# Performance work log

Measured on AMD Instinct MI355X. Metric: run time of the kernel, lower is better.

The kernel has to match this reference:

```python
import jax, jax.numpy as jnp
import numpy as np

B, S, R, H, NH, HD = 32, 1026, 256, 1024, 16, 64

def setup_inputs() -> dict:
    key = jax.random.key(0)
    ks = jax.random.split(key, 8)
    sc = 0.02
    return {
        "q_low": jax.random.normal(ks[0], (B, S, R), jnp.float32),
        "k_low": jax.random.normal(ks[1], (B, S, R), jnp.float32),
        "v_low": jax.random.normal(ks[2], (B, S, R), jnp.float32),
        "Wq": jax.random.normal(ks[3], (R, H), jnp.float32) * sc,
        "bq": jnp.zeros((H,), jnp.float32),
        "Wk": jax.random.normal(ks[4], (R, H), jnp.float32) * sc,
        "bk": jnp.zeros((H,), jnp.float32),
        "Wv": jax.random.normal(ks[5], (R, H), jnp.float32) * sc,
        "bv": jnp.zeros((H,), jnp.float32),
        "Wo_down": jax.random.normal(ks[6], (H, R), jnp.float32) * sc,
    }

def reference(q_low, k_low, v_low, Wq, bq, Wk, bk, Wv, bv, Wo_down):
    # Up-project low-rank activations to full Q, K, V: [B,S,R] @ [R,H] -> [B,S,H]
    q = q_low @ Wq + bq
    k = k_low @ Wk + bk
    v = v_low @ Wv + bv
    # split heads: [B,S,NH,HD] -> [B,NH,S,HD]
    def split(x):
        return x.reshape(B, S, NH, HD).transpose(0, 2, 1, 3)
    qh, kh, vh = split(q), split(k), split(v)
    scores = jnp.einsum('bhqd,bhkd->bhqk', qh, kh) / jnp.sqrt(jnp.float32(HD))
    probs = jax.nn.softmax(scores, axis=-1)  # dropout p=0
    ctx = jnp.einsum('bhqk,bhkd->bhqd', probs, vh)
    ctx = ctx.transpose(0, 2, 1, 3).reshape(B, S, H)
    # Down-project with low-rank activation (gelu)
    out_low = jax.nn.gelu(ctx @ Wo_down, approximate=False)
    return out_low
```

## Files before the change

kernel.cpp:

```cpp
#include <hip/hip_runtime.h>
#include <hip/hip_bf16.h>
#include <math.h>

using short8   = __attribute__((ext_vector_type(8))) short;
using floatx4  = __attribute__((ext_vector_type(4))) float;
using floatx16 = __attribute__((ext_vector_type(16))) float;

#define B_N  32
#define S_N  1026
#define R_N  256
#define H_N  1024
#define NH_N 16
#define HD_N 64
#define SP_N 1088
#define KTILES 17
#define CS_LD 136

__device__ __forceinline__ float bf2f(__hip_bfloat16 x) { return __bfloat162float(x); }
__device__ __forceinline__ __hip_bfloat16 f2bf(float x) { return __float2bfloat16(x); }

__device__ __forceinline__ float fast_exp2(float x) {
#if __has_builtin(__builtin_amdgcn_exp2f)
    return __builtin_amdgcn_exp2f(x);
#else
    return exp2f(x);
#endif
}

__device__ __forceinline__ unsigned cvtpk(float lo, float hi_) {
    unsigned r;
    asm("v_cvt_pk_bf16_f32 %0, %1, %2" : "=v"(r) : "v"(lo), "v"(hi_));
    return r;
}

__device__ __forceinline__ void gl_lds16(const void* g, void* l) {
    __builtin_amdgcn_global_load_lds(
        (const __attribute__((address_space(1))) unsigned int*)g,
        (__attribute__((address_space(3))) unsigned int*)l, 16, 0, 0);
}

__device__ __forceinline__ int xcd_swz(int o, int nwg) {
    return ((nwg & 7) == 0) ? ((o & 7) * (nwg >> 3) + (o >> 3)) : o;
}

__device__ __forceinline__ short8 cvt8(const float* __restrict__ p) {
    floatx4 a = *(const floatx4*)p;
    floatx4 b = *(const floatx4*)(p + 4);
    short8 o;
    __hip_bfloat16* op = (__hip_bfloat16*)&o;
    op[0] = f2bf(a[0]); op[1] = f2bf(a[1]); op[2] = f2bf(a[2]); op[3] = f2bf(a[3]);
    op[4] = f2bf(b[0]); op[5] = f2bf(b[1]); op[6] = f2bf(b[2]); op[7] = f2bf(b[3]);
    return o;
}

__global__ __launch_bounds__(256) void transpose3_kernel(
    const float* __restrict__ a, const float* __restrict__ b, const float* __restrict__ c,
    __hip_bfloat16* __restrict__ oa, __hip_bfloat16* __restrict__ ob,
    __hip_bfloat16* __restrict__ oc, int K, int N) {
    __shared__ __hip_bfloat16 t[32][33];
    const float* in = (blockIdx.z == 0) ? a : (blockIdx.z == 1) ? b : c;
    __hip_bfloat16* out = (blockIdx.z == 0) ? oa : (blockIdx.z == 1) ? ob : oc;
    const int k0 = blockIdx.x * 32, n0 = blockIdx.y * 32;
    const int tx = threadIdx.x & 31, ty = threadIdx.x >> 5;
#pragma unroll
    for (int j = 0; j < 32; j += 8)
        t[ty + j][tx] = f2bf(in[(size_t)(k0 + ty + j) * N + n0 + tx]);
    __syncthreads();
#pragma unroll
    for (int j = 0; j < 32; j += 8)
        out[(size_t)(n0 + ty + j) * K + k0 + tx] = t[tx][ty + j];
}

__global__ __launch_bounds__(256) void transpose_kernel(const float* __restrict__ in,
                                                        __hip_bfloat16* __restrict__ out,
                                                        int K, int N) {
    __shared__ __hip_bfloat16 t[32][33];
    const int k0 = blockIdx.x * 32, n0 = blockIdx.y * 32;
    const int tx = threadIdx.x & 31, ty = threadIdx.x >> 5;
#pragma unroll
    for (int j = 0; j < 32; j += 8)
        t[ty + j][tx] = f2bf(in[(size_t)(k0 + ty + j) * N + n0 + tx]);
    __syncthreads();
#pragma unroll
    for (int j = 0; j < 32; j += 8)
        out[(size_t)(n0 + ty + j) * K + k0 + tx] = t[tx][ty + j];
}

__global__ __launch_bounds__(256) void cvtx_kernel(
    const float* __restrict__ q, const float* __restrict__ k, const float* __restrict__ v,
    __hip_bfloat16* __restrict__ oq, __hip_bfloat16* __restrict__ ok,
    __hip_bfloat16* __restrict__ ov, int n8) {
    int idx = blockIdx.x * 256 + threadIdx.x;
    if (idx >= n8) return;
    const float* s = (blockIdx.y == 0) ? q : (blockIdx.y == 1) ? k : v;
    __hip_bfloat16* d = (blockIdx.y == 0) ? oq : (blockIdx.y == 1) ? ok : ov;
    *(short8*)(d + (size_t)idx * 8) = cvt8(s + (size_t)idx * 8);
}

__global__ void padv_kernel(__hip_bfloat16* __restrict__ Vt, int total) {
    int idx = blockIdx.x * 256 + threadIdx.x;
    if (idx < total) {
        int p  = idx % (SP_N - S_N);
        int rd = idx / (SP_N - S_N);
        Vt[(size_t)rd * SP_N + S_N + p] = f2bf(0.f);
    }
}

__global__ __launch_bounds__(256) void qkvproj_kernel(
    const __hip_bfloat16* __restrict__ Xq, const __hip_bfloat16* __restrict__ Xk,
    const __hip_bfloat16* __restrict__ Xv,
    const __hip_bfloat16* __restrict__ WqT, const __hip_bfloat16* __restrict__ WkT,
    const __hip_bfloat16* __restrict__ WvT,
    const float* __restrict__ bq, const float* __restrict__ bk,
    const float* __restrict__ bv,
    __hip_bfloat16* __restrict__ Qc, __hip_bfloat16* __restrict__ Kc,
    __hip_bfloat16* __restrict__ Vc, int Mc, float qscale) {
    __shared__ char smem[34816];
    typedef __hip_bfloat16 (*AB_t)[128][32];
    AB_t As = (AB_t)smem;
    AB_t Bs = (AB_t)(smem + 16384);
    __hip_bfloat16* Cs = (__hip_bfloat16*)smem;

    const int nx = gridDim.x;
    const int nwg = nx * 8 * 3;
    const int o = blockIdx.x + nx * (blockIdx.y + 8 * blockIdx.z);
    const int tlin = xcd_swz(o, nwg);
    const int ty = tlin & 7;
    const int rest = tlin >> 3;
    const int tx = rest % nx, tz = rest / nx;

    const __hip_bfloat16* X  = (tz == 0) ? Xq  : (tz == 1) ? Xk  : Xv;
    const __hip_bfloat16* WT = (tz == 0) ? WqT : (tz == 1) ? WkT : WvT;
    const float* bias        = (tz == 0) ? bq  : (tz == 1) ? bk  : bv;
    __hip_bfloat16* out      = (tz == 0) ? Qc  : (tz == 1) ? Kc  : Vc;
    const float oscale = (tz == 0) ? qscale : 1.0f;
    const int mode = (tz == 2);

    const int tid  = threadIdx.x;
    const int wave = tid >> 6, lane = tid & 63;
    const int quad = lane >> 4, l16 = lane & 15;
    const int tm = tx * 128, tn = ty * 128;
    const int mw = (wave >> 1) * 64, nw = (wave & 1) * 64;
    const int lr = lane >> 2;
    const int sc4 = (lane & 3) ^ (lr & 3);

    floatx4 acc[4][4] = {};

    auto stage = [&](int bb, int kk) {
#pragma unroll
        for (int s16 = 0; s16 < 2; ++s16) {
            int row = wave * 32 + s16 * 16;
            int gm = tm + row + lr; if (gm >= Mc) gm = Mc - 1;
            gl_lds16(X + (size_t)gm * R_N + kk + sc4 * 8, &As[bb][row][0]);
            gl_lds16(WT + (size_t)(tn + row + lr) * R_N + kk + sc4 * 8, &Bs[bb][row][0]);
        }
    };

    stage(0, 0);
    __syncthreads();

    for (int t = 0; t < R_N / 32; ++t) {
        const int bb = t & 1;
        if (t + 1 < R_N / 32) stage(bb ^ 1, (t + 1) * 32);
        short8 af[4], bfr[4];
#pragma unroll
        for (int mb = 0; mb < 4; ++mb) {
            int row = mw + mb * 16 + l16;
            af[mb] = *(const short8*)((const char*)&As[bb][row][0] + ((quad ^ (row & 3)) << 4));
        }
#pragma unroll
        for (int nb = 0; nb < 4; ++nb) {
            int row = nw + nb * 16 + l16;
            bfr[nb] = *(const short8*)((const char*)&Bs[bb][row][0] + ((quad ^ (row & 3)) << 4));
        }
        if (mode == 0) {
#pragma unroll
            for (int mb = 0; mb < 4; ++mb)
#pragma unroll
                for (int nb = 0; nb < 4; ++nb)
                    acc[mb][nb] = __builtin_amdgcn_mfma_f32_16x16x32_bf16(af[mb], bfr[nb], acc[mb][nb], 0, 0, 0);
        } else {
#pragma unroll
            for (int mb = 0; mb < 4; ++mb)
#pragma unroll
                for (int nb = 0; nb < 4; ++nb)
                    acc[mb][nb] = __builtin_amdgcn_mfma_f32_16x16x32_bf16(bfr[nb], af[mb], acc[mb][nb], 0, 0, 0);
        }
        __syncthreads();
    }

    if (mode == 0) {
#pragma unroll
        for (int mb = 0; mb < 4; ++mb)
#pragma unroll
            for (int nb = 0; nb < 4; ++nb) {
                int j = nw + nb * 16 + l16;
                float bv_ = bias[tn + j];
#pragma unroll
                for (int r = 0; r < 4; ++r) {
                    int i = mw + mb * 16 + quad * 4 + r;
                    Cs[i * CS_LD + j] = f2bf(oscale * (acc[mb][nb][r] + bv_));
                }
            }
    } else {
#pragma unroll
        for (int mb = 0; mb < 4; ++mb)
#pragma unroll
            for (int nb = 0; nb < 4; ++nb)
#pragma unroll
                for (int r = 0; r < 4; ++r) {
                    int i = nw + nb * 16 + quad * 4 + r;
                    int j = mw + mb * 16 + l16;
                    Cs[i * CS_LD + j] = f2bf(acc[mb][nb][r] + bias[tn + i]);
                }
    }
    __syncthreads();

    const int i = tid >> 1, half = tid & 1;
    if (mode == 0) {
        int m = tm + i;
        if (m < Mc) {
            int bl = m / S_N, s = m - bl * S_N;
            int h = (tn >> 6) + half;
            size_t ob = ((size_t)((bl * NH_N + h) * S_N + s)) * HD_N;
            const __hip_bfloat16* src = Cs + i * CS_LD + half * 64;
#pragma unroll
            for (int j = 0; j < 8; ++j)
                *(short8*)(out + ob + j * 8) = *(const short8*)(src + j * 8);
        }
    } else {
        int n = tn + i;
        int h = n >> 6, d = n & 63;
        const __hip_bfloat16* src = Cs + i * CS_LD + half * 64;
#pragma unroll
        for (int j = 0; j < 8; ++j) {
            int m0 = tm + half * 64 + j * 8;
            if (m0 >= Mc) continue;
            short8 w = *(const short8*)(src + j * 8);
            int bl = m0 / S_N, s0 = m0 - bl * S_N;
            size_t ob = ((size_t)((bl * NH_N + h) * HD_N + d)) * SP_N;
            if (s0 + 8 <= S_N) {
                const unsigned* wp = (const unsigned*)&w;
#pragma unroll
                for (int k = 0; k < 4; ++k)
                    *(unsigned*)(out + ob + s0 + 2 * k) = wp[k];
            } else {
                const __hip_bfloat16* we = (const __hip_bfloat16*)&w;
#pragma unroll
                for (int e = 0; e < 8; ++e) {
                    int m = m0 + e;
                    int bl2 = m / S_N, s2 = m - bl2 * S_N;
                    out[((size_t)((bl2 * NH_N + h) * HD_N + d)) * SP_N + s2] = we[e];
                }
            }
        }
    }
}

__global__ __launch_bounds__(256, 3) void attn_kernel(
    const __hip_bfloat16* __restrict__ Qh,
    const __hip_bfloat16* __restrict__ Kh,
    const __hip_bfloat16* __restrict__ Vt,
    __hip_bfloat16* __restrict__ ctx) {
    __shared__ __hip_bfloat16 Kl[2][64][64];
    __shared__ __hip_bfloat16 Vl[2][64][64];

    const int ny = gridDim.y;
    const int nwg = gridDim.x * ny;
    const int o = blockIdx.x + gridDim.x * blockIdx.y;
    const int tlin = xcd_swz(o, nwg);
    const int bh = tlin / ny;
    const int q0 = (tlin % ny) * 128;

    const int tid = threadIdx.x;
    const int wave = tid >> 6, lane = tid & 63;
    const int c = lane & 31, hi = lane >> 5, c7 = c & 7;
    const size_t base  = (size_t)bh * S_N * HD_N;
    const size_t vbase = (size_t)bh * HD_N * SP_N;

    const int lr = lane >> 3;
    const int sc = (lane & 7) ^ lr;

    const short ONE = 0x3F80;
    const short8 onesb = {ONE, ONE, ONE, ONE, ONE, ONE, ONE, ONE};

    short8 qf[4];
    {
        int qrow = q0 + wave * 32 + c;
        if (qrow > S_N - 1) qrow = S_N - 1;
        const __hip_bfloat16* qp = Qh + base + (size_t)qrow * HD_N + hi * 8;
#pragma unroll
        for (int i = 0; i < 4; ++i) qf[i] = *(const short8*)(qp + 16 * i);
    }

    floatx16 oacc[2] = {};
    floatx16 rsacc = {};

    auto stage = [&](int bb, int kt) {
#pragma unroll
        for (int j = 0; j < 2; ++j) {
            int r = 16 * wave + 8 * j + lr;
            int krow = kt + r;
            if (krow > S_N - 1) krow = S_N - 1;
            gl_lds16(Kh + base + (size_t)krow * HD_N + sc * 8,
                     &Kl[bb][16 * wave + 8 * j][0]);
            gl_lds16(Vt + vbase + (size_t)r * SP_N + kt + sc * 8,
                     &Vl[bb][16 * wave + 8 * j][0]);
        }
    };

    stage(0, 0);
    __syncthreads();

    int bb = 0;
    for (int t = 0; t < KTILES; ++t) {
        const int kt = t * 64;
        if (t + 1 < KTILES) stage(bb ^ 1, kt + 64);
        const bool last = (kt + 64 > S_N);

        short8 pa[2][2];
#pragma unroll
        for (int sub = 0; sub < 2; ++sub) {
            floatx16 sacc = {};
            __builtin_amdgcn_s_setprio(1);
#pragma unroll
            for (int i = 0; i < 4; ++i) {
                short8 kf = *(const short8*)&Kl[bb][32 * sub + c][(((2 * i + hi) ^ c7) << 3)];
                sacc = __builtin_amdgcn_mfma_f32_32x32x16_bf16(kf, qf[i], sacc, 0, 0, 0);
            }
            __builtin_amdgcn_s_setprio(0);
            float ps[16];
            if (!last) {
#pragma unroll
                for (int r = 0; r < 16; ++r) ps[r] = fast_exp2(sacc[r]);
            } else {
#pragma unroll
                for (int r = 0; r < 16; ++r) {
                    int key = kt + 32 * sub + (r & 3) + 8 * (r >> 2) + 4 * hi;
                    ps[r] = (key < S_N) ? fast_exp2(sacc[r]) : 0.f;
                }
            }
#pragma unroll
            for (int step = 0; step < 2; ++step) {
                unsigned w0 = cvtpk(ps[8 * step + 0], ps[8 * step + 1]);
                unsigned w1 = cvtpk(ps[8 * step + 2], ps[8 * step + 3]);
                unsigned w2 = cvtpk(ps[8 * step + 4], ps[8 * step + 5]);
                unsigned w3 = cvtpk(ps[8 * step + 6], ps[8 * step + 7]);
                asm("v_permlane32_swap_b32 %0, %1" : "+v"(w0), "+v"(w2));
                asm("v_permlane32_swap_b32 %0, %1" : "+v"(w1), "+v"(w3));
                union { unsigned u[4]; short8 s; } fu;
                fu.u[0] = w0; fu.u[1] = w1; fu.u[2] = w2; fu.u[3] = w3;
                pa[sub][step] = fu.s;
            }
        }

        __builtin_amdgcn_s_setprio(1);
#pragma unroll
        for (int db = 0; db < 2; ++db)
#pragma unroll
            for (int sub = 0; sub < 2; ++sub)
#pragma unroll
                for (int step = 0; step < 2; ++step) {
                    short8 vf = *(const short8*)
                        &Vl[bb][32 * db + c][((((sub * 2 + step) * 2 + hi) ^ c7) << 3)];
                    oacc[db] = __builtin_amdgcn_mfma_f32_32x32x16_bf16(pa[sub][step], vf, oacc[db], 0, 0, 0);
                }
#pragma unroll
        for (int sub = 0; sub < 2; ++sub)
#pragma unroll
            for (int step = 0; step < 2; ++step)
                rsacc = __builtin_amdgcn_mfma_f32_32x32x16_bf16(pa[sub][step], onesb, rsacc, 0, 0, 0);
        __builtin_amdgcn_s_setprio(0);

        __syncthreads();
        bb ^= 1;
    }

    const int bl = bh / NH_N, h = bh - bl * NH_N;
    const int srow0 = q0 + wave * 32;
#pragma unroll
    for (int r = 0; r < 16; ++r) {
        int q = (r & 3) + 8 * (r >> 2) + 4 * hi;
        int s = srow0 + q;
        if (s < S_N) {
            float rr = 1.0f / rsacc[r];
            size_t o2 = ((size_t)(bl * S_N + s)) * H_N + h * HD_N + c;
            ctx[o2]      = f2bf(oacc[0][r] * rr);
            ctx[o2 + 32] = f2bf(oacc[1][r] * rr);
        }
    }
}

__global__ __launch_bounds__(256) void dproj_kernel(
    const __hip_bfloat16* __restrict__ X,
    const __hip_bfloat16* __restrict__ WT,
    float* __restrict__ out,
    int Mc) {
    __shared__ char smem[49152];
    typedef __hip_bfloat16 (*A_t)[64][64];
    typedef __hip_bfloat16 (*B_t)[128][64];
    A_t As = (A_t)smem;
    B_t Bs = (B_t)(smem + 16384);
    float* Csf = (float*)smem;

    const int nx = (Mc + 63) >> 6;
    const int tlin = xcd_swz(blockIdx.x, gridDim.x);
    if (tlin >= nx * 2) return;
    const int ty = tlin & 1, tx = tlin >> 1;

    const int tid  = threadIdx.x;
    const int wave = tid >> 6, lane = tid & 63;
    const int quad = lane >> 4, l16 = lane & 15;
    const int tm = tx * 64, tn = ty * 128;
    const int mw = (wave >> 1) * 32, nw = (wave & 1) * 64;
    const int lr = lane >> 3;
    const int sc = (lane & 7) ^ lr;

    floatx4 acc[2][4] = {};

    auto stage = [&](int bb, int kk) {
#pragma unroll
        for (int s8 = 0; s8 < 2; ++s8) {
            int row = wave * 16 + s8 * 8;
            int gm = tm + row + lr; if (gm >= Mc) gm = Mc - 1;
            gl_lds16(X + (size_t)gm * H_N + kk + sc * 8, &As[bb][row][0]);
        }
#pragma unroll
        for (int s8 = 0; s8 < 4; ++s8) {
            int row = wave * 32 + s8 * 8;
            gl_lds16(WT + (size_t)(tn + row + lr) * H_N + kk + sc * 8, &Bs[bb][row][0]);
        }
    };

    stage(0, 0);
    __syncthreads();

    for (int t = 0; t < H_N / 64; ++t) {
        const int bb = t & 1;
        if (t + 1 < H_N / 64) stage(bb ^ 1, (t + 1) * 64);
        short8 af[2][2], bfr[4][2];
#pragma unroll
        for (int mb = 0; mb < 2; ++mb) {
            int row = mw + mb * 16 + l16;
            const char* rp = (const char*)&As[bb][row][0];
#pragma unroll
            for (int k2 = 0; k2 < 2; ++k2)
                af[mb][k2] = *(const short8*)(rp + ((((k2 * 4 + quad)) ^ (row & 7)) << 4));
        }
#pragma unroll
        for (int nb = 0; nb < 4; ++nb) {
            int row = nw + nb * 16 + l16;
            const char* rp = (const char*)&Bs[bb][row][0];
#pragma unroll
            for (int k2 = 0; k2 < 2; ++k2)
                bfr[nb][k2] = *(const short8*)(rp + ((((k2 * 4 + quad)) ^ (row & 7)) << 4));
        }
#pragma unroll
        for (int mb = 0; mb < 2; ++mb)
#pragma unroll
            for (int nb = 0; nb < 4; ++nb) {
                acc[mb][nb] = __builtin_amdgcn_mfma_f32_16x16x32_bf16(af[mb][0], bfr[nb][0], acc[mb][nb], 0, 0, 0);
                acc[mb][nb] = __builtin_amdgcn_mfma_f32_16x16x32_bf16(af[mb][1], bfr[nb][1], acc[mb][nb], 0, 0, 0);
            }
        __syncthreads();
    }

#pragma unroll
    for (int mb = 0; mb < 2; ++mb)
#pragma unroll
        for (int nb = 0; nb < 4; ++nb)
#pragma unroll
            for (int r = 0; r < 4; ++r) {
                int i = mw + mb * 16 + quad * 4 + r;
                int j = nw + nb * 16 + l16;
                float x = acc[mb][nb][r];
                Csf[i * CS_LD + j] = 0.5f * x * (1.0f + erff(x * 0.70710678118654752f));
            }
    __syncthreads();

    {
        const int i = tid >> 2, q32 = tid & 3;
        int m = tm + i;
        if (m < Mc) {
            const float* src = Csf + i * CS_LD + q32 * 32;
            float* dst = out + (size_t)m * R_N + tn + q32 * 32;
#pragma unroll
            for (int jj = 0; jj < 8; ++jj)
                *(floatx4*)(dst + jj * 4) = *(const floatx4*)(src + jj * 4);
        }
    }
}

extern "C" void kernel_launch(void* const* d_in, const int* in_sizes, int n_in,
                              void* d_out, int out_size, void* d_ws, size_t ws_size,
                              hipStream_t stream) {
    const float* q_low = (const float*)d_in[0];
    const float* k_low = (const float*)d_in[1];
    const float* v_low = (const float*)d_in[2];
    const float* Wq    = (const float*)d_in[3];
    const float* bq    = (const float*)d_in[4];
    const float* Wk    = (const float*)d_in[5];
    const float* bk    = (const float*)d_in[6];
    const float* Wv    = (const float*)d_in[7];
    const float* bv    = (const float*)d_in[8];
    const float* Wo    = (const float*)d_in[9];
    float* out = (float*)d_out;
    (void)in_sizes; (void)n_in; (void)out_size;

    const float QSCALE = 0.125f * 1.44269504088896f;
    const size_t SZ_W = (size_t)H_N * R_N * 2;

    int C = 32;
    while (C > 1) {
        size_t qk = (size_t)C * NH_N * S_N * HD_N * 2;
        size_t vv = (size_t)C * NH_N * HD_N * SP_N * 2;
        size_t cx = (size_t)C * S_N * H_N * 2;
        if (4 * SZ_W + 2 * qk + vv + cx <= ws_size) break;
        C >>= 1;
    }

    char* ws = (char*)d_ws;
    const size_t SZ_QK = (size_t)C * NH_N * S_N * HD_N * 2;
    const size_t SZ_V  = (size_t)C * NH_N * HD_N * SP_N * 2;
    __hip_bfloat16* WqT = (__hip_bfloat16*)(ws);
    __hip_bfloat16* WkT = (__hip_bfloat16*)(ws + SZ_W);
    __hip_bfloat16* WvT = (__hip_bfloat16*)(ws + 2 * SZ_W);
    __hip_bfloat16* WoT = (__hip_bfloat16*)(ws + 3 * SZ_W);
    __hip_bfloat16* Qc  = (__hip_bfloat16*)(ws + 4 * SZ_W);
    __hip_bfloat16* Kc  = (__hip_bfloat16*)(ws + 4 * SZ_W + SZ_QK);
    __hip_bfloat16* Vc  = (__hip_bfloat16*)(ws + 4 * SZ_W + 2 * SZ_QK);
    __hip_bfloat16* ctc = (__hip_bfloat16*)(ws + 4 * SZ_W + 2 * SZ_QK + SZ_V);

    {
        dim3 tg(R_N / 32, H_N / 32, 3);
        transpose3_kernel<<<tg, 256, 0, stream>>>(Wq, Wk, Wv, WqT, WkT, WvT, R_N, H_N);
        dim3 to(H_N / 32, R_N / 32);
        transpose_kernel<<<to, 256, 0, stream>>>(Wo, WoT, H_N, R_N);
    }

    {
        int total = C * NH_N * HD_N * (SP_N - S_N);
        padv_kernel<<<(total + 255) / 256, 256, 0, stream>>>(Vc, total);
    }

    for (int c0 = 0; c0 < B_N; c0 += C) {
        const int Mc = C * S_N;
        const size_t xoff = (size_t)c0 * S_N * R_N;

        __hip_bfloat16* Xq = ctc;
        __hip_bfloat16* Xk = ctc + (size_t)Mc * R_N;
        __hip_bfloat16* Xv = ctc + 2 * (size_t)Mc * R_N;
        {
            int n8 = Mc * R_N / 8;
            dim3 cg((n8 + 255) / 256, 3);
            cvtx_kernel<<<cg, 256, 0, stream>>>(q_low + xoff, k_low + xoff, v_low + xoff,
                                                Xq, Xk, Xv, n8);
        }

        dim3 pg((Mc + 127) / 128, H_N / 128, 3);
        qkvproj_kernel<<<pg, 256, 0, stream>>>(Xq, Xk, Xv, WqT, WkT, WvT,
                                               bq, bk, bv, Qc, Kc, Vc, Mc, QSCALE);

        dim3 ag(C * NH_N, (S_N + 127) / 128);
        attn_kernel<<<ag, 256, 0, stream>>>(Qc, Kc, Vc, ctc);

        int nxd = (Mc + 63) / 64;
        int dg1 = ((nxd * 2 + 7) / 8) * 8;
        dproj_kernel<<<dg1, 256, 0, stream>>>(ctc, WoT, out + xoff, Mc);
    }
}
```

Baseline: 518.1 us.

## Process two query tiles per wave in attention to reuse K/V LDS fragments

The attention kernel now uses 2 waves (128 threads) per block instead of 4. Each wave handles 64 query rows as two 32-row groups, so every K and V fragment read from LDS feeds two MFMAs instead of one. Each wave also stages twice as many K/V rows. This halves LDS read traffic per query row and raises MFMA density. The cost is doubled accumulator and register pressure, fewer waves per block to hide latency, and launch bounds that change occupancy.

```diff
diff --git a/kernel.cpp b/kernel.cpp
--- a/kernel.cpp
+++ b/kernel.cpp
@@ -257,7 +257,7 @@
     }
 }
 
-__global__ __launch_bounds__(256, 3) void attn_kernel(
+__global__ __launch_bounds__(128, 2) void attn_kernel(
     const __hip_bfloat16* __restrict__ Qh,
     const __hip_bfloat16* __restrict__ Kh,
     const __hip_bfloat16* __restrict__ Vt,
@@ -284,28 +284,29 @@
     const short ONE = 0x3F80;
     const short8 onesb = {ONE, ONE, ONE, ONE, ONE, ONE, ONE, ONE};
 
-    short8 qf[4];
-    {
-        int qrow = q0 + wave * 32 + c;
+    short8 qf[2][4];
+#pragma unroll
+    for (int g = 0; g < 2; ++g) {
+        int qrow = q0 + wave * 64 + g * 32 + c;
         if (qrow > S_N - 1) qrow = S_N - 1;
         const __hip_bfloat16* qp = Qh + base + (size_t)qrow * HD_N + hi * 8;
 #pragma unroll
-        for (int i = 0; i < 4; ++i) qf[i] = *(const short8*)(qp + 16 * i);
-    }
-
-    floatx16 oacc[2] = {};
-    floatx16 rsacc = {};
+        for (int i = 0; i < 4; ++i) qf[g][i] = *(const short8*)(qp + 16 * i);
+    }
+
+    floatx16 oacc[2][2] = {};
+    floatx16 rsacc[2] = {};
 
     auto stage = [&](int bb, int kt) {
 #pragma unroll
-        for (int j = 0; j < 2; ++j) {
-            int r = 16 * wave + 8 * j + lr;
+        for (int j = 0; j < 4; ++j) {
+            int r = 32 * wave + 8 * j + lr;
             int krow = kt + r;
             if (krow > S_N - 1) krow = S_N - 1;
             gl_lds16(Kh + base + (size_t)krow * HD_N + sc * 8,
-                     &Kl[bb][16 * wave + 8 * j][0]);
+                     &Kl[bb][32 * wave + 8 * j][0]);
             gl_lds16(Vt + vbase + (size_t)r * SP_N + kt + sc * 8,
-                     &Vl[bb][16 * wave + 8 * j][0]);
+                     &Vl[bb][32 * wave + 8 * j][0]);
         }
     };
 
@@ -318,39 +319,44 @@
         if (t + 1 < KTILES) stage(bb ^ 1, kt + 64);
         const bool last = (kt + 64 > S_N);
 
-        short8 pa[2][2];
+        short8 pa[2][2][2];
 #pragma unroll
         for (int sub = 0; sub < 2; ++sub) {
-            floatx16 sacc = {};
-            __builtin_amdgcn_s_setprio(1);
-#pragma unroll
-            for (int i = 0; i < 4; ++i) {
-                short8 kf = *(const short8*)&Kl[bb][32 * sub + c][(((2 * i + hi) ^ c7) << 3)];
-                sacc = __builtin_amdgcn_mfma_f32_32x32x16_bf16(kf, qf[i], sacc, 0, 0, 0);
-            }
-            __builtin_amdgcn_s_setprio(0);
-            float ps[16];
-            if (!last) {
-#pragma unroll
-                for (int r = 0; r < 16; ++r) ps[r] = fast_exp2(sacc[r]);
-            } else {
-#pragma unroll
-                for (int r = 0; r < 16; ++r) {
-                    int key = kt + 32 * sub + (r & 3) + 8 * (r >> 2) + 4 * hi;
-                    ps[r] = (key < S_N) ? fast_exp2(sacc[r]) : 0.f;
+            short8 kf[4];
+#pragma unroll
+            for (int i = 0; i < 4; ++i)
+                kf[i] = *(const short8*)&Kl[bb][32 * sub + c][(((2 * i + hi) ^ c7) << 3)];
+#pragma unroll
+            for (int g = 0; g < 2; ++g) {
+                floatx16 sacc = {};
+                __builtin_amdgcn_s_setprio(1);
+#pragma unroll
+                for (int i = 0; i < 4; ++i)
+                    sacc = __builtin_amdgcn_mfma_f32_32x32x16_bf16(kf[i], qf[g][i], sacc, 0, 0, 0);
+                __builtin_amdgcn_s_setprio(0);
+                float ps[16];
+                if (!last) {
+#pragma unroll
+                    for (int r = 0; r < 16; ++r) ps[r] = fast_exp2(sacc[r]);
+                } else {
+#pragma unroll
+                    for (int r = 0; r < 16; ++r) {
+                        int key = kt + 32 * sub + (r & 3) + 8 * (r >> 2) + 4 * hi;
+                        ps[r] = (key < S_N) ? fast_exp2(sacc[r]) : 0.f;
+                    }
                 }
-            }
-#pragma unroll
-            for (int step = 0; step < 2; ++step) {
-                unsigned w0 = cvtpk(ps[8 * step + 0], ps[8 * step + 1]);
-                unsigned w1 = cvtpk(ps[8 * step + 2], ps[8 * step + 3]);
-                unsigned w2 = cvtpk(ps[8 * step + 4], ps[8 * step + 5]);
-                unsigned w3 = cvtpk(ps[8 * step + 6], ps[8 * step + 7]);
-                asm("v_permlane32_swap_b32 %0, %1" : "+v"(w0), "+v"(w2));
-                asm("v_permlane32_swap_b32 %0, %1" : "+v"(w1), "+v"(w3));
-                union { unsigned u[4]; short8 s; } fu;
-                fu.u[0] = w0; fu.u[1] = w1; fu.u[2] = w2; fu.u[3] = w3;
-                pa[sub][step] = fu.s;
+#pragma unroll
+                for (int step = 0; step < 2; ++step) {
+                    unsigned w0 = cvtpk(ps[8 * step + 0], ps[8 * step + 1]);
+                    unsigned w1 = cvtpk(ps[8 * step + 2], ps[8 * step + 3]);
+                    unsigned w2 = cvtpk(ps[8 * step + 4], ps[8 * step + 5]);
+                    unsigned w3 = cvtpk(ps[8 * step + 6], ps[8 * step + 7]);
+                    asm("v_permlane32_swap_b32 %0, %1" : "+v"(w0), "+v"(w2));
+                    asm("v_permlane32_swap_b32 %0, %1" : "+v"(w1), "+v"(w3));
+                    union { unsigned u[4]; short8 s; } fu;
+                    fu.u[0] = w0; fu.u[1] = w1; fu.u[2] = w2; fu.u[3] = w3;
+                    pa[g][sub][step] = fu.s;
+                }
             }
         }
 
@@ -363,13 +369,17 @@
                 for (int step = 0; step < 2; ++step) {
                     short8 vf = *(const short8*)
                         &Vl[bb][32 * db + c][((((sub * 2 + step) * 2 + hi) ^ c7) << 3)];
-                    oacc[db] = __builtin_amdgcn_mfma_f32_32x32x16_bf16(pa[sub][step], vf, oacc[db], 0, 0, 0);
+#pragma unroll
+                    for (int g = 0; g < 2; ++g)
+                        oacc[g][db] = __builtin_amdgcn_mfma_f32_32x32x16_bf16(pa[g][sub][step], vf, oacc[g][db], 0, 0, 0);
                 }
 #pragma unroll
         for (int sub = 0; sub < 2; ++sub)
 #pragma unroll
             for (int step = 0; step < 2; ++step)
-                rsacc = __builtin_amdgcn_mfma_f32_32x32x16_bf16(pa[sub][step], onesb, rsacc, 0, 0, 0);
+#pragma unroll
+                for (int g = 0; g < 2; ++g)
+                    rsacc[g] = __builtin_amdgcn_mfma_f32_32x32x16_bf16(pa[g][sub][step], onesb, rsacc[g], 0, 0, 0);
         __builtin_amdgcn_s_setprio(0);
 
         __syncthreads();
@@ -377,16 +387,19 @@
     }
 
     const int bl = bh / NH_N, h = bh - bl * NH_N;
-    const int srow0 = q0 + wave * 32;
-#pragma unroll
-    for (int r = 0; r < 16; ++r) {
-        int q = (r & 3) + 8 * (r >> 2) + 4 * hi;
-        int s = srow0 + q;
-        if (s < S_N) {
-            float rr = 1.0f / rsacc[r];
-            size_t o2 = ((size_t)(bl * S_N + s)) * H_N + h * HD_N + c;
-            ctx[o2]      = f2bf(oacc[0][r] * rr);
-            ctx[o2 + 32] = f2bf(oacc[1][r] * rr);
+#pragma unroll
+    for (int g = 0; g < 2; ++g) {
+        const int srow0 = q0 + wave * 64 + g * 32;
+#pragma unroll
+        for (int r = 0; r < 16; ++r) {
+            int q = (r & 3) + 8 * (r >> 2) + 4 * hi;
+            int s = srow0 + q;
+            if (s < S_N) {
+                float rr = 1.0f / rsacc[g][r];
+                size_t o2 = ((size_t)(bl * S_N + s)) * H_N + h * HD_N + c;
+                ctx[o2]      = f2bf(oacc[g][0][r] * rr);
+                ctx[o2 + 32] = f2bf(oacc[g][1][r] * rr);
+            }
         }
     }
 }
@@ -562,7 +575,7 @@
                                                bq, bk, bv, Qc, Kc, Vc, Mc, QSCALE);
 
         dim3 ag(C * NH_N, (S_N + 127) / 128);
-        attn_kernel<<<ag, 256, 0, stream>>>(Qc, Kc, Vc, ctc);
+        attn_kernel<<<ag, 128, 0, stream>>>(Qc, Kc, Vc, ctc);
 
         int nxd = (Mc + 63) / 64;
         int dg1 = ((nxd * 2 + 7) / 8) * 8;
```

Measured after the change: 557.9 us. 7.7% more time.

## Enlarge QKV projection tile to 256x128 with 512-thread blocks

Applied to the files above, without the earlier changes.

The QKV up-projection GEMM now uses 256-row M tiles and 8 waves per block, so each staged weight (B) tile is reused across twice as many activation rows. To fit the larger A tile in shared memory, the epilogue writes results through the C staging buffer in two passes of 128 rows each, with extra barriers. This cuts redundant weight loads and the block count, at the cost of more LDS per block, possible lower occupancy, and a serialized two-pass epilogue.

```diff
diff --git a/kernel.cpp b/kernel.cpp
--- a/kernel.cpp
+++ b/kernel.cpp
@@ -106,7 +106,7 @@
     }
 }
 
-__global__ __launch_bounds__(256) void qkvproj_kernel(
+__global__ __launch_bounds__(512) void qkvproj_kernel(
     const __hip_bfloat16* __restrict__ Xq, const __hip_bfloat16* __restrict__ Xk,
     const __hip_bfloat16* __restrict__ Xv,
     const __hip_bfloat16* __restrict__ WqT, const __hip_bfloat16* __restrict__ WkT,
@@ -115,10 +115,11 @@
     const float* __restrict__ bv,
     __hip_bfloat16* __restrict__ Qc, __hip_bfloat16* __restrict__ Kc,
     __hip_bfloat16* __restrict__ Vc, int Mc, float qscale) {
-    __shared__ char smem[34816];
-    typedef __hip_bfloat16 (*AB_t)[128][32];
-    AB_t As = (AB_t)smem;
-    AB_t Bs = (AB_t)(smem + 16384);
+    __shared__ char smem[49152];
+    typedef __hip_bfloat16 (*A_t)[256][32];
+    typedef __hip_bfloat16 (*B_t)[128][32];
+    A_t As = (A_t)smem;
+    B_t Bs = (B_t)(smem + 32768);
     __hip_bfloat16* Cs = (__hip_bfloat16*)smem;
 
     const int nx = gridDim.x;
@@ -139,8 +140,9 @@
     const int tid  = threadIdx.x;
     const int wave = tid >> 6, lane = tid & 63;
     const int quad = lane >> 4, l16 = lane & 15;
-    const int tm = tx * 128, tn = ty * 128;
-    const int mw = (wave >> 1) * 64, nw = (wave & 1) * 64;
+    const int tm = tx * 256, tn = ty * 128;
+    const int wm = wave >> 1, wn = wave & 1;
+    const int mw = wm * 64, nw = wn * 64;
     const int lr = lane >> 2;
     const int sc4 = (lane & 3) ^ (lr & 3);
 
@@ -152,6 +154,9 @@
             int row = wave * 32 + s16 * 16;
             int gm = tm + row + lr; if (gm >= Mc) gm = Mc - 1;
             gl_lds16(X + (size_t)gm * R_N + kk + sc4 * 8, &As[bb][row][0]);
+        }
+        {
+            int row = wave * 16;
             gl_lds16(WT + (size_t)(tn + row + lr) * R_N + kk + sc4 * 8, &Bs[bb][row][0]);
         }
     };
@@ -189,71 +194,78 @@
         __syncthreads();
     }
 
-    if (mode == 0) {
-#pragma unroll
-        for (int mb = 0; mb < 4; ++mb)
-#pragma unroll
-            for (int nb = 0; nb < 4; ++nb) {
-                int j = nw + nb * 16 + l16;
-                float bv_ = bias[tn + j];
-#pragma unroll
-                for (int r = 0; r < 4; ++r) {
-                    int i = mw + mb * 16 + quad * 4 + r;
-                    Cs[i * CS_LD + j] = f2bf(oscale * (acc[mb][nb][r] + bv_));
+#pragma unroll
+    for (int pass = 0; pass < 2; ++pass) {
+        if ((wm >> 1) == pass) {
+            if (mode == 0) {
+#pragma unroll
+                for (int mb = 0; mb < 4; ++mb)
+#pragma unroll
+                    for (int nb = 0; nb < 4; ++nb) {
+                        int j = nw + nb * 16 + l16;
+                        float bv_ = bias[tn + j];
+#pragma unroll
+                        for (int r = 0; r < 4; ++r) {
+                            int li = (wm & 1) * 64 + mb * 16 + quad * 4 + r;
+                            Cs[li * CS_LD + j] = f2bf(oscale * (acc[mb][nb][r] + bv_));
+                        }
+                    }
+            } else {
+#pragma unroll
+                for (int mb = 0; mb < 4; ++mb)
+#pragma unroll
+                    for (int nb = 0; nb < 4; ++nb)
+#pragma unroll
+                        for (int r = 0; r < 4; ++r) {
+                            int i = nw + nb * 16 + quad * 4 + r;
+                            int jc = (wm & 1) * 64 + mb * 16 + l16;
+                            Cs[i * CS_LD + jc] = f2bf(acc[mb][nb][r] + bias[tn + i]);
+                        }
+            }
+        }
+        __syncthreads();
+
+        const int i = tid >> 2, qq = tid & 3;
+        if (mode == 0) {
+            int m = tm + pass * 128 + i;
+            if (m < Mc) {
+                int bl = m / S_N, s = m - bl * S_N;
+                int h = (tn + qq * 32) >> 6;
+                int d0 = (qq * 32) & 63;
+                size_t ob = ((size_t)((bl * NH_N + h) * S_N + s)) * HD_N + d0;
+                const __hip_bfloat16* src = Cs + i * CS_LD + qq * 32;
+#pragma unroll
+                for (int j = 0; j < 4; ++j)
+                    *(short8*)(out + ob + j * 8) = *(const short8*)(src + j * 8);
+            }
+        } else {
+            int n = tn + i;
+            int h = n >> 6, d = n & 63;
+            const __hip_bfloat16* src = Cs + i * CS_LD + qq * 32;
+#pragma unroll
+            for (int j = 0; j < 4; ++j) {
+                int m0 = tm + pass * 128 + qq * 32 + j * 8;
+                if (m0 >= Mc) continue;
+                short8 w = *(const short8*)(src + j * 8);
+                int bl = m0 / S_N, s0 = m0 - bl * S_N;
+                size_t ob = ((size_t)((bl * NH_N + h) * HD_N + d)) * SP_N;
+                if (s0 + 8 <= S_N) {
+                    const unsigned* wp = (const unsigned*)&w;
+#pragma unroll
+                    for (int k = 0; k < 4; ++k)
+                        *(unsigned*)(out + ob + s0 + 2 * k) = wp[k];
+                } else {
+                    const __hip_bfloat16* we = (const __hip_bfloat16*)&w;
+#pragma unroll
+                    for (int e = 0; e < 8; ++e) {
+                        int m = m0 + e;
+                        int bl2 = m / S_N, s2 = m - bl2 * S_N;
+                        out[((size_t)((bl2 * NH_N + h) * HD_N + d)) * SP_N + s2] = we[e];
+                    }
                 }
             }
-    } else {
-#pragma unroll
-        for (int mb = 0; mb < 4; ++mb)
-#pragma unroll
-            for (int nb = 0; nb < 4; ++nb)
-#pragma unroll
-                for (int r = 0; r < 4; ++r) {
-                    int i = nw + nb * 16 + quad * 4 + r;
-                    int j = mw + mb * 16 + l16;
-                    Cs[i * CS_LD + j] = f2bf(acc[mb][nb][r] + bias[tn + i]);
-                }
-    }
-    __syncthreads();
-
-    const int i = tid >> 1, half = tid & 1;
-    if (mode == 0) {
-        int m = tm + i;
-        if (m < Mc) {
-            int bl = m / S_N, s = m - bl * S_N;
-            int h = (tn >> 6) + half;
-            size_t ob = ((size_t)((bl * NH_N + h) * S_N + s)) * HD_N;
-            const __hip_bfloat16* src = Cs + i * CS_LD + half * 64;
-#pragma unroll
-            for (int j = 0; j < 8; ++j)
-                *(short8*)(out + ob + j * 8) = *(const short8*)(src + j * 8);
-        }
-    } else {
-        int n = tn + i;
-        int h = n >> 6, d = n & 63;
-        const __hip_bfloat16* src = Cs + i * CS_LD + half * 64;
-#pragma unroll
-        for (int j = 0; j < 8; ++j) {
-            int m0 = tm + half * 64 + j * 8;
-            if (m0 >= Mc) continue;
-            short8 w = *(const short8*)(src + j * 8);
-            int bl = m0 / S_N, s0 = m0 - bl * S_N;
-            size_t ob = ((size_t)((bl * NH_N + h) * HD_N + d)) * SP_N;
-            if (s0 + 8 <= S_N) {
-                const unsigned* wp = (const unsigned*)&w;
-#pragma unroll
-                for (int k = 0; k < 4; ++k)
-                    *(unsigned*)(out + ob + s0 + 2 * k) = wp[k];
-            } else {
-                const __hip_bfloat16* we = (const __hip_bfloat16*)&w;
-#pragma unroll
-                for (int e = 0; e < 8; ++e) {
-                    int m = m0 + e;
-                    int bl2 = m / S_N, s2 = m - bl2 * S_N;
-                    out[((size_t)((bl2 * NH_N + h) * HD_N + d)) * SP_N + s2] = we[e];
-                }
-            }
-        }
+        }
+        __syncthreads();
     }
 }
 
@@ -557,8 +569,8 @@
                                                 Xq, Xk, Xv, n8);
         }
 
-        dim3 pg((Mc + 127) / 128, H_N / 128, 3);
-        qkvproj_kernel<<<pg, 256, 0, stream>>>(Xq, Xk, Xv, WqT, WkT, WvT,
+        dim3 pg((Mc + 255) / 256, H_N / 128, 3);
+        qkvproj_kernel<<<pg, 512, 0, stream>>>(Xq, Xk, Xv, WqT, WkT, WvT,
                                                bq, bk, bv, Qc, Kc, Vc, Mc, QSCALE);
 
         dim3 ag(C * NH_N, (S_N + 127) / 128);
```

New measurement: 553.0 us. +6.7%, slower.
